# Optimization experiments

Hardware: AMD Instinct MI355X
Metric: run time of the kernel (lower is better)

## Reference

```python
import jax, jax.numpy as jnp
import numpy as np

N, D, NUM_CLASSES = 8192, 128, 1000


def setup_inputs() -> dict:
    key = jax.random.key(0)
    ka, kb, kt = jax.random.split(key, 3)
    fa = jax.random.normal(ka, (N, D), dtype=jnp.float32)
    fb = jax.random.normal(kb, (N, D), dtype=jnp.float32)
    # L2-normalize as in standard contrastive setups (CLIP-style)
    fa = fa / jnp.linalg.norm(fa, axis=-1, keepdims=True)
    fb = fb / jnp.linalg.norm(fb, axis=-1, keepdims=True)
    targets = jax.random.randint(kt, (N,), 0, NUM_CLASSES, dtype=jnp.int64 if jax.config.jax_enable_x64 else jnp.int32)
    T = jnp.array([100.0], dtype=jnp.float32)  # logit scale
    return {
        "T": T,
        "local_features_a": fa,
        "local_features_b": fb,
        "global_targets": targets,
        "training": 1,
    }


def reference(T, local_features_a, local_features_b, global_targets, training):
    # world_size = 1: local features ARE the global features; the chunked
    # online-softmax reduction in the original is mathematically identical
    # to a stable logsumexp over the full logits row (max is detached, so
    # gradients also match).
    eq = (global_targets[:, None] == global_targets[None, :]).astype(jnp.float32)  # [N, N] positive mask
    target_sum = jnp.sum(eq, axis=-1)  # [N]

    def one_direction(fa, fb):
        logits = T * (fa @ fb.T)  # [N, N]
        weighted = -jnp.sum(eq * logits, axis=-1)            # sum of -logits over positives
        lse = jax.nn.logsumexp(logits, axis=-1)              # online-softmax global reduction
        per_row = weighted / target_sum + lse                # [N]
        return jnp.mean(per_row)

    loss_i = one_direction(local_features_a, local_features_b)
    loss_t = one_direction(local_features_b, local_features_a)
    return (loss_i + loss_t) / 2.0
```

## Files before the change

kernel.cpp:

```cpp
#include <hip/hip_runtime.h>
#include <hip/hip_bf16.h>

#define CN 8192
#define CD 128
#define NCLS 1000
#define MAXC 256
#define CLS_BLOCKS 250
#define TILE_BLOCKS 512

typedef __attribute__((ext_vector_type(8))) short bf16x8;
typedef __attribute__((ext_vector_type(4))) float f32x4;

#define WS_B_OFF     0x200000u
#define WS_CNT_OFF   0x400000u
#define WS_EXTRA_OFF 0x401000u
#define WS_ROWE_OFF  0x402000u
#define WS_COLE_OFF  0x40A000u
#define WS_ACC_OFF   0x412000u
#define WS_DONE_OFF  0x412004u
#define WS_BKT_OFF   0x413000u
#define WS_ROWP_OFF  0x490000u
#define WS_COLP_OFF  0x890000u
#define WS_FAST_BYTES 0xA90000u
#define WS_ZERO_BYTES 0x12100u

__device__ inline unsigned short f2bf(float f) {
    unsigned int u = __float_as_uint(f);
    return (unsigned short)((u + 0x7FFFu + ((u >> 16) & 1u)) >> 16);
}

__global__ void convert_kernel(const float* __restrict__ fa, const float* __restrict__ fb,
                               unsigned short* __restrict__ Abf, unsigned short* __restrict__ Bbf,
                               const int* __restrict__ tgt,
                               int* __restrict__ cnt, unsigned short* __restrict__ bucket) {
    int gid = blockIdx.x * 256 + threadIdx.x;
    int i = gid * 4;
    const float* src = blockIdx.y == 0 ? fa : fb;
    unsigned short* dst = blockIdx.y == 0 ? Abf : Bbf;
    float4 v = *reinterpret_cast<const float4*>(src + i);
    ushort4 o;
    o.x = f2bf(v.x); o.y = f2bf(v.y); o.z = f2bf(v.z); o.w = f2bf(v.w);
    *reinterpret_cast<ushort4*>(dst + i) = o;

    if (blockIdx.y == 0 && (gid & 31) == 0) {
        int row = gid >> 5;
        int t = tgt[row];
        int slot = atomicAdd(&cnt[t], 1);
        if (slot < MAXC) bucket[t * MAXC + slot] = (unsigned short)row;
    }
}

__global__ __launch_bounds__(256) void mega_kernel(
    const float* __restrict__ Tptr,
    const unsigned short* __restrict__ Abf,
    const unsigned short* __restrict__ Bbf,
    const float* __restrict__ fa, const float* __restrict__ fb,
    const int* __restrict__ cnt, const unsigned short* __restrict__ bucket,
    float* __restrict__ extra,
    float* __restrict__ rowE, float* __restrict__ colE,
    float* __restrict__ rowPart, float* __restrict__ colPart,
    int store_mode)
{
    __shared__ __align__(16) unsigned short sA[128 * 128];
    __shared__ __align__(16) unsigned short sB[2][64 * 128];
    __shared__ float colRed[2][4][64];

    const int bid  = blockIdx.x;
    const int tid  = threadIdx.x;
    const int lane = tid & 63;
    const int w    = tid >> 6;

    if (bid < CLS_BLOCKS) {
        const int c = bid * 4 + w;
        const int n = cnt[c];
        const int m = n < MAXC ? n : MAXC;
        const float* src = lane < 32 ? fa : fb;
        const int d = (lane & 31) * 4;
        float ax = 0.f, ay = 0.f, az = 0.f, aw = 0.f;
        for (int s = 0; s < m; ++s) {
            int row = bucket[c * MAXC + s];
            float4 v = *reinterpret_cast<const float4*>(src + (size_t)row * CD + d);
            ax += v.x; ay += v.y; az += v.z; aw += v.w;
        }
        float bx_ = __shfl_xor(ax, 32), by_ = __shfl_xor(ay, 32);
        float bz_ = __shfl_xor(az, 32), bw_ = __shfl_xor(aw, 32);
        float p = ax * bx_ + ay * by_ + az * bz_ + aw * bw_;
        #pragma unroll
        for (int off = 1; off < 32; off <<= 1) p += __shfl_xor(p, off);
        if (lane == 0) extra[c] = n > 0 ? (-2.0f * Tptr[0] * p / (float)n) : 0.f;
        return;
    }

    const int tb    = bid - CLS_BLOCKS;
    const int bx    = tb & 7;
    const int by    = tb >> 3;
    const int brow  = by * 128;
    const int cbase = bx * 1024;
    const float T   = Tptr[0];
    const float Tl2 = T * 1.44269504088896340736f;

    #pragma unroll
    for (int it = 0; it < 8; ++it) {
        int idx = it * 256 + tid;
        int r = idx >> 4, q = idx & 15;
        const unsigned short* src = Abf + (size_t)(brow + r) * CD + ((q ^ (r & 7)) * 8);
        __builtin_amdgcn_global_load_lds((const __attribute__((address_space(1))) void*)src,
                                         (__attribute__((address_space(3))) void*)&sA[idx * 8],
                                         16, 0, 0);
    }
    #pragma unroll
    for (int it = 0; it < 4; ++it) {
        int idx = it * 256 + tid;
        int r = idx >> 4, q = idx & 15;
        const unsigned short* src = Bbf + (size_t)(cbase + r) * CD + ((q ^ (r & 7)) * 8);
        __builtin_amdgcn_global_load_lds((const __attribute__((address_space(1))) void*)src,
                                         (__attribute__((address_space(3))) void*)&sB[0][idx * 8],
                                         16, 0, 0);
    }
    __syncthreads();

    const int colg = lane & 15;
    const int rowg = lane >> 4;

    float rE[2][4] = {{0.f, 0.f, 0.f, 0.f}, {0.f, 0.f, 0.f, 0.f}};

    for (int ct = 0; ct < 16; ++ct) {
        const int cur = ct & 1;
        if (ct < 15) {
            int bcolN = cbase + (ct + 1) * 64;
            #pragma unroll
            for (int it = 0; it < 4; ++it) {
                int idx = it * 256 + tid;
                int r = idx >> 4, q = idx & 15;
                const unsigned short* src = Bbf + (size_t)(bcolN + r) * CD + ((q ^ (r & 7)) * 8);
                __builtin_amdgcn_global_load_lds((const __attribute__((address_space(1))) void*)src,
                                                 (__attribute__((address_space(3))) void*)&sB[cur ^ 1][idx * 8],
                                                 16, 0, 0);
            }
        }

        f32x4 acc[2][4];
        #pragma unroll
        for (int m = 0; m < 2; ++m)
            #pragma unroll
            for (int n = 0; n < 4; ++n)
                acc[m][n] = (f32x4){0.f, 0.f, 0.f, 0.f};

        #pragma unroll
        for (int kk = 0; kk < 4; ++kk) {
            bf16x8 af[2], bfr[4];
            #pragma unroll
            for (int m = 0; m < 2; ++m) {
                int r = w * 32 + m * 16 + colg;
                int slot = (kk * 4 + rowg) ^ (r & 7);
                af[m] = *reinterpret_cast<const bf16x8*>(&sA[r * 128 + slot * 8]);
            }
            #pragma unroll
            for (int n = 0; n < 4; ++n) {
                int r = n * 16 + colg;
                int slot = (kk * 4 + rowg) ^ (r & 7);
                bfr[n] = *reinterpret_cast<const bf16x8*>(&sB[cur][r * 128 + slot * 8]);
            }
            #pragma unroll
            for (int m = 0; m < 2; ++m)
                #pragma unroll
                for (int n = 0; n < 4; ++n)
                    acc[m][n] = __builtin_amdgcn_mfma_f32_16x16x32_bf16(af[m], bfr[n], acc[m][n], 0, 0, 0);
        }

        float cE[4] = {0.f, 0.f, 0.f, 0.f};
        #pragma unroll
        for (int m = 0; m < 2; ++m)
            #pragma unroll
            for (int n = 0; n < 4; ++n)
                #pragma unroll
                for (int j = 0; j < 4; ++j) {
                    float e = exp2f(__builtin_fmaf(acc[m][n][j], Tl2, -Tl2));
                    rE[m][j] += e;
                    cE[n]    += e;
                }

        #pragma unroll
        for (int n = 0; n < 4; ++n) {
            float e = cE[n];
            e += __shfl_xor(e, 16);
            e += __shfl_xor(e, 32);
            if (rowg == 0) colRed[cur][w][n * 16 + colg] = e;
        }
        __syncthreads();
        if (tid < 64) {
            float s = colRed[cur][0][tid] + colRed[cur][1][tid]
                    + colRed[cur][2][tid] + colRed[cur][3][tid];
            int col = cbase + ct * 64 + tid;
            if (store_mode) colPart[(size_t)by * CN + col] = s;
            else            atomicAdd(&colE[col], s);
        }
    }

    #pragma unroll
    for (int m = 0; m < 2; ++m)
        #pragma unroll
        for (int j = 0; j < 4; ++j) {
            float e = rE[m][j];
            #pragma unroll
            for (int off = 1; off < 16; off <<= 1) e += __shfl_xor(e, off);
            if (colg == 0) {
                int row = brow + w * 32 + m * 16 + rowg * 4 + j;
                if (store_mode) rowPart[(size_t)bx * CN + row] = e;
                else            atomicAdd(&rowE[row], e);
            }
        }
}

__global__ __launch_bounds__(256) void finalize_kernel(
    const float* __restrict__ Tptr,
    const float* __restrict__ rowE, const float* __restrict__ colE,
    const float* __restrict__ rowPart, const float* __restrict__ colPart,
    const float* __restrict__ extra,
    float* __restrict__ wsAcc, unsigned int* __restrict__ wsDone,
    float* __restrict__ out, int store_mode)
{
    __shared__ float red[4];
    const int tid = threadIdx.x;
    int i = blockIdx.x * 256 + tid;
    const float T = Tptr[0];
    float v = 0.f;
    if (i < CN) {
        float se;
        if (store_mode) {
            se = 0.f;
            #pragma unroll
            for (int p = 0; p < 8; ++p) se += rowPart[(size_t)p * CN + i];
        } else se = rowE[i];
        v = T + logf(se);
    } else if (i < 2 * CN) {
        int c = i - CN;
        float se;
        if (store_mode) {
            se = 0.f;
            #pragma unroll 4
            for (int p = 0; p < 64; ++p) se += colPart[(size_t)p * CN + c];
        } else se = colE[c];
        v = T + logf(se);
    } else if (i < 2 * CN + NCLS) {
        v = extra[i - 2 * CN];
    }
    #pragma unroll
    for (int off = 1; off < 64; off <<= 1) v += __shfl_xor(v, off);
    if ((tid & 63) == 0) red[tid >> 6] = v;
    __syncthreads();
    if (tid == 0) {
        float tot = red[0] + red[1] + red[2] + red[3];
        atomicAdd(wsAcc, tot);
        __threadfence();
        unsigned int old = atomicAdd(wsDone, 1u);
        if (old == gridDim.x - 1) {
            float total = atomicAdd(wsAcc, 0.0f);
            out[0] = total * (1.0f / (2.0f * (float)CN));
        }
    }
}

extern "C" void kernel_launch(void* const* d_in, const int* in_sizes, int n_in,
                              void* d_out, int out_size, void* d_ws, size_t ws_size,
                              hipStream_t stream) {
    const float* T  = (const float*)d_in[0];
    const float* fa = (const float*)d_in[1];
    const float* fb = (const float*)d_in[2];
    const int* tgt  = (const int*)d_in[3];
    float* out      = (float*)d_out;

    char* ws = (char*)d_ws;
    unsigned short* Abf = (unsigned short*)ws;
    unsigned short* Bbf = (unsigned short*)(ws + WS_B_OFF);
    int*   cnt    = (int*)(ws + WS_CNT_OFF);
    float* extra  = (float*)(ws + WS_EXTRA_OFF);
    float* rowE   = (float*)(ws + WS_ROWE_OFF);
    float* colE   = (float*)(ws + WS_COLE_OFF);
    float* wsAcc  = (float*)(ws + WS_ACC_OFF);
    unsigned int* wsDone = (unsigned int*)(ws + WS_DONE_OFF);
    unsigned short* bucket = (unsigned short*)(ws + WS_BKT_OFF);
    float* rowPart = (float*)(ws + WS_ROWP_OFF);
    float* colPart = (float*)(ws + WS_COLP_OFF);

    const int store_mode = (ws_size >= WS_FAST_BYTES) ? 1 : 0;

    hipMemsetAsync(ws + WS_CNT_OFF, 0, WS_ZERO_BYTES, stream);

    convert_kernel<<<dim3(CN * CD / (256 * 4), 2), 256, 0, stream>>>(fa, fb, Abf, Bbf, tgt, cnt, bucket);

    mega_kernel<<<CLS_BLOCKS + TILE_BLOCKS, 256, 0, stream>>>(
        T, Abf, Bbf, fa, fb, cnt, bucket, extra,
        rowE, colE, rowPart, colPart, store_mode);

    finalize_kernel<<<(2 * CN + NCLS + 255) / 256, 256, 0, stream>>>(
        T, rowE, colE, rowPart, colPart, extra, wsAcc, wsDone, out, store_mode);
}
```

Before: 126.1 us.

## Hold A fragments in registers, drop sA LDS, double tile-block count

The A tile is now loaded straight from global memory into registers once per block instead of being staged in shared memory, which frees 32KB of LDS per block and allows more resident blocks (launch bounds set to 4 per SM). The column range per block is halved (512 columns) and the tile-block count doubled to 1024 to expose more parallelism, with finalize summing 16 row partials instead of 8. The exp/accumulate epilogue is rewritten with packed two-wide float FMAs. This trades more blocks, atomics and partial writes, plus higher register pressure from the held A fragments, for less LDS traffic and better occupancy.

Result: faster. 119.5 us (-5.2%).

```diff
diff --git a/kernel.cpp b/kernel.cpp
--- a/kernel.cpp
+++ b/kernel.cpp
@@ -6,10 +6,11 @@
 #define NCLS 1000
 #define MAXC 256
 #define CLS_BLOCKS 250
-#define TILE_BLOCKS 512
+#define TILE_BLOCKS 1024
 
 typedef __attribute__((ext_vector_type(8))) short bf16x8;
 typedef __attribute__((ext_vector_type(4))) float f32x4;
+typedef __attribute__((ext_vector_type(2))) float f32x2;
 
 #define WS_B_OFF     0x200000u
 #define WS_CNT_OFF   0x400000u
@@ -50,7 +51,7 @@
     }
 }
 
-__global__ __launch_bounds__(256) void mega_kernel(
+__global__ __launch_bounds__(256, 4) void mega_kernel(
     const float* __restrict__ Tptr,
     const unsigned short* __restrict__ Abf,
     const unsigned short* __restrict__ Bbf,
@@ -61,7 +62,6 @@
     float* __restrict__ rowPart, float* __restrict__ colPart,
     int store_mode)
 {
-    __shared__ __align__(16) unsigned short sA[128 * 128];
     __shared__ __align__(16) unsigned short sB[2][64 * 128];
     __shared__ float colRed[2][4][64];
 
@@ -92,22 +92,27 @@
     }
 
     const int tb    = bid - CLS_BLOCKS;
-    const int bx    = tb & 7;
-    const int by    = tb >> 3;
+    const int bx    = tb & 15;
+    const int by    = tb >> 4;
     const int brow  = by * 128;
-    const int cbase = bx * 1024;
-    const float T   = Tptr[0];
-    const float Tl2 = T * 1.44269504088896340736f;
-
+    const int cbase = bx * 512;
+    const float T    = Tptr[0];
+    const float Tl2  = T * 1.44269504088896340736f;
+    const f32x2 Tl2v  = {Tl2, Tl2};
+    const f32x2 nTl2v = {-Tl2, -Tl2};
+
+    const int colg = lane & 15;
+    const int rowg = lane >> 4;
+
+    bf16x8 afr[2][4];
     #pragma unroll
-    for (int it = 0; it < 8; ++it) {
-        int idx = it * 256 + tid;
-        int r = idx >> 4, q = idx & 15;
-        const unsigned short* src = Abf + (size_t)(brow + r) * CD + ((q ^ (r & 7)) * 8);
-        __builtin_amdgcn_global_load_lds((const __attribute__((address_space(1))) void*)src,
-                                         (__attribute__((address_space(3))) void*)&sA[idx * 8],
-                                         16, 0, 0);
-    }
+    for (int m = 0; m < 2; ++m) {
+        const unsigned short* arow = Abf + (size_t)(brow + w * 32 + m * 16 + colg) * CD + rowg * 8;
+        #pragma unroll
+        for (int kk = 0; kk < 4; ++kk)
+            afr[m][kk] = *reinterpret_cast<const bf16x8*>(arow + kk * 32);
+    }
+
     #pragma unroll
     for (int it = 0; it < 4; ++it) {
         int idx = it * 256 + tid;
@@ -119,14 +124,11 @@
     }
     __syncthreads();
 
-    const int colg = lane & 15;
-    const int rowg = lane >> 4;
-
-    float rE[2][4] = {{0.f, 0.f, 0.f, 0.f}, {0.f, 0.f, 0.f, 0.f}};
-
-    for (int ct = 0; ct < 16; ++ct) {
+    f32x2 rE2[2][2] = {{{0.f, 0.f}, {0.f, 0.f}}, {{0.f, 0.f}, {0.f, 0.f}}};
+
+    for (int ct = 0; ct < 8; ++ct) {
         const int cur = ct & 1;
-        if (ct < 15) {
+        if (ct < 7) {
             int bcolN = cbase + (ct + 1) * 64;
             #pragma unroll
             for (int it = 0; it < 4; ++it) {
@@ -148,13 +150,7 @@
 
         #pragma unroll
         for (int kk = 0; kk < 4; ++kk) {
-            bf16x8 af[2], bfr[4];
-            #pragma unroll
-            for (int m = 0; m < 2; ++m) {
-                int r = w * 32 + m * 16 + colg;
-                int slot = (kk * 4 + rowg) ^ (r & 7);
-                af[m] = *reinterpret_cast<const bf16x8*>(&sA[r * 128 + slot * 8]);
-            }
+            bf16x8 bfr[4];
             #pragma unroll
             for (int n = 0; n < 4; ++n) {
                 int r = n * 16 + colg;
@@ -165,24 +161,30 @@
             for (int m = 0; m < 2; ++m)
                 #pragma unroll
                 for (int n = 0; n < 4; ++n)
-                    acc[m][n] = __builtin_amdgcn_mfma_f32_16x16x32_bf16(af[m], bfr[n], acc[m][n], 0, 0, 0);
-        }
-
-        float cE[4] = {0.f, 0.f, 0.f, 0.f};
+                    acc[m][n] = __builtin_amdgcn_mfma_f32_16x16x32_bf16(afr[m][kk], bfr[n], acc[m][n], 0, 0, 0);
+        }
+
+        f32x2 cE2[4] = {{0.f, 0.f}, {0.f, 0.f}, {0.f, 0.f}, {0.f, 0.f}};
         #pragma unroll
         for (int m = 0; m < 2; ++m)
             #pragma unroll
-            for (int n = 0; n < 4; ++n)
-                #pragma unroll
-                for (int j = 0; j < 4; ++j) {
-                    float e = exp2f(__builtin_fmaf(acc[m][n][j], Tl2, -Tl2));
-                    rE[m][j] += e;
-                    cE[n]    += e;
-                }
+            for (int n = 0; n < 4; ++n) {
+                f32x4 a4 = acc[m][n];
+                f32x2 d01 = {a4[0], a4[1]};
+                f32x2 d23 = {a4[2], a4[3]};
+                f32x2 t01 = __builtin_elementwise_fma(d01, Tl2v, nTl2v);
+                f32x2 t23 = __builtin_elementwise_fma(d23, Tl2v, nTl2v);
+                f32x2 e01 = {exp2f(t01.x), exp2f(t01.y)};
+                f32x2 e23 = {exp2f(t23.x), exp2f(t23.y)};
+                rE2[m][0] += e01;
+                rE2[m][1] += e23;
+                cE2[n] += e01;
+                cE2[n] += e23;
+            }
 
         #pragma unroll
         for (int n = 0; n < 4; ++n) {
-            float e = cE[n];
+            float e = cE2[n].x + cE2[n].y;
             e += __shfl_xor(e, 16);
             e += __shfl_xor(e, 32);
             if (rowg == 0) colRed[cur][w][n * 16 + colg] = e;
@@ -200,14 +202,22 @@
     #pragma unroll
     for (int m = 0; m < 2; ++m)
         #pragma unroll
-        for (int j = 0; j < 4; ++j) {
-            float e = rE[m][j];
-            #pragma unroll
-            for (int off = 1; off < 16; off <<= 1) e += __shfl_xor(e, off);
+        for (int jp = 0; jp < 2; ++jp) {
+            f32x2 e = rE2[m][jp];
+            #pragma unroll
+            for (int off = 1; off < 16; off <<= 1) {
+                e.x += __shfl_xor(e.x, off);
+                e.y += __shfl_xor(e.y, off);
+            }
             if (colg == 0) {
-                int row = brow + w * 32 + m * 16 + rowg * 4 + j;
-                if (store_mode) rowPart[(size_t)bx * CN + row] = e;
-                else            atomicAdd(&rowE[row], e);
+                int row0 = brow + w * 32 + m * 16 + rowg * 4 + jp * 2;
+                if (store_mode) {
+                    rowPart[(size_t)bx * CN + row0]     = e.x;
+                    rowPart[(size_t)bx * CN + row0 + 1] = e.y;
+                } else {
+                    atomicAdd(&rowE[row0],     e.x);
+                    atomicAdd(&rowE[row0 + 1], e.y);
+                }
             }
         }
 }
@@ -230,7 +240,7 @@
         if (store_mode) {
             se = 0.f;
             #pragma unroll
-            for (int p = 0; p < 8; ++p) se += rowPart[(size_t)p * CN + i];
+            for (int p = 0; p < 16; ++p) se += rowPart[(size_t)p * CN + i];
         } else se = rowE[i];
         v = T + logf(se);
     } else if (i < 2 * CN) {
```
